# Kernel tuning notes

Measured on AMD Instinct MI355X. Metric: run time of the kernel, lower is better.

The kernel has to match this reference:

```python
import jax, jax.numpy as jnp
import numpy as np

N = 50000      # nodes
E = 500000     # edges
G = 8          # graphs in batch
IN = 128       # in_dim
HID = 64       # hidden_dim_graph == hidden_dim1
H = 2          # num_heads
C = 2          # n_classes
SLOPE = 0.2    # DGL GATConv leaky_relu negative slope


def setup_inputs() -> dict:
    key = jax.random.key(0)
    ks = jax.random.split(key, 16)
    s = lambda k, sh, fan: (jax.random.normal(k, sh, jnp.float32) / np.float32(np.sqrt(fan)))
    return {
        "h_n": jax.random.normal(ks[0], (N, IN), jnp.float32),
        "src": jax.random.randint(ks[1], (E,), 0, N),
        "dst": jax.random.randint(ks[2], (E,), 0, N),
        "graph_ids": jnp.sort(jax.random.randint(ks[3], (N,), 0, G)),
        # GATConv layer 1: fc [IN, H*HID], attn vectors [H, HID]
        "W_fc1": s(ks[4], (IN, H * HID), IN),
        "attn_l1": s(ks[5], (H, HID), HID),
        "attn_r1": s(ks[6], (H, HID), HID),
        # GATConv layer 2: fc [HID, H*HID]
        "W_fc2": s(ks[7], (HID, H * HID), HID),
        "attn_l2": s(ks[8], (H, HID), HID),
        "attn_r2": s(ks[9], (H, HID), HID),
        # gate nn: Linear(HID, 1)
        "w_gate": s(ks[10], (HID, 1), HID),
        "b_gate": jnp.zeros((1,), jnp.float32),
        # classifier MLP
        "W_c1": s(ks[11], (HID, HID), HID),
        "b_c1": jnp.zeros((HID,), jnp.float32),
        "W_c2": s(ks[12], (HID, C), HID),
        "b_c2": jnp.zeros((C,), jnp.float32),
    }


def _gat_conv(h, src, dst, W_fc, attn_l, attn_r):
    # h: [N, D_in] -> out: [N, H, HID]
    feat = (h @ W_fc).reshape(N, H, HID)
    el = (feat * attn_l).sum(-1)                 # [N, H]
    er = (feat * attn_r).sum(-1)                 # [N, H]
    e = jax.nn.leaky_relu(el[src] + er[dst], SLOPE)   # [E, H]
    # edge softmax over incoming edges per destination node
    m = jax.ops.segment_max(e, dst, num_segments=N)   # [N, H]
    ex = jnp.exp(e - m[dst])                     # [E, H]
    den = jax.ops.segment_sum(ex, dst, num_segments=N)
    alpha = ex / jnp.where(den == 0, 1.0, den)[dst]
    # message passing: sum_e alpha_e * feat[src_e]
    return jax.ops.segment_sum(alpha[:, :, None] * feat[src], dst, num_segments=N)


def _segment_softmax(x, ids, num_segments):
    m = jax.ops.segment_max(x, ids, num_segments=num_segments)
    ex = jnp.exp(x - m[ids])
    den = jax.ops.segment_sum(ex, ids, num_segments=num_segments)
    return ex / jnp.where(den == 0, 1.0, den)[ids]


def reference(h_n, src, dst, graph_ids, W_fc1, attn_l1, attn_r1, W_fc2, attn_l2,
              attn_r2, w_gate, b_gate, W_c1, b_c1, W_c2, b_c2):
    h = jax.nn.relu(_gat_conv(h_n, src, dst, W_fc1, attn_l1, attn_r1)).mean(axis=1)
    h = jax.nn.relu(_gat_conv(h, src, dst, W_fc2, attn_l2, attn_r2)).mean(axis=1)
    # global attention pooling (gate MLP + per-graph softmax + weighted sum)
    gate = (h @ w_gate + b_gate)[:, 0]                 # [N]
    a = _segment_softmax(gate, graph_ids, G)[:, None]  # [N, 1]
    hg = jax.ops.segment_sum(a * h, graph_ids, num_segments=G)  # [G, HID]
    # classifier head (dropout is identity in eval mode)
    a2 = hg @ W_c1 + b_c1
    a3 = a2 @ W_c2 + b_c2
    return (jax.nn.sigmoid(a3), a, hg)
```

## Files before the change

kernel.cpp:

```cpp
#include <hip/hip_runtime.h>
#include <hip/hip_bf16.h>

#define NN 50000
#define EE 500000
#define GG 8
#define INDIM 128
#define HID 64
#define NH 2
#define PB 32
#define TMM 32
#define CAP 32
#define NBF ((NN + TMM - 1) / TMM)
#define EPB ((EE + NBF - 1) / NBF)

typedef __bf16 bf16x4 __attribute__((ext_vector_type(4)));
typedef __bf16 bf16x8 __attribute__((ext_vector_type(8)));
typedef float  f32x4  __attribute__((ext_vector_type(4)));

__device__ inline unsigned short f2bf(float f) {
    unsigned int u = __float_as_uint(f);
    unsigned int r = (u + 0x7FFFu + ((u >> 16) & 1u)) >> 16;
    return (unsigned short)r;
}
__device__ inline unsigned int pack_bf16x2(float lo, float hi) {
    return (unsigned int)f2bf(lo) | ((unsigned int)f2bf(hi) << 16);
}
__device__ inline int lower_bound_g(const int* __restrict__ gids, int target, int N) {
    int lo = 0, hi = N;
    while (lo < hi) { int mid = (lo + hi) >> 1; if (gids[mid] < target) lo = mid + 1; else hi = mid; }
    return lo;
}

__global__ __launch_bounds__(256) void prep_kernel(
        const float* __restrict__ W1, const float* __restrict__ W2,
        unsigned short* __restrict__ Wf1, unsigned short* __restrict__ Wf2,
        unsigned int* __restrict__ zero_base) {
    int idx = blockIdx.x * 256 + threadIdx.x;
    const int ZN = GG + GG + GG * 64 + NN;
    if (idx < ZN) zero_base[idx] = 0u;
    if (idx < 128 * 128) {
        int c = idx >> 7, r = idx & 127;
        int ks = r >> 5, g = (r >> 3) & 3, e = r & 7;
        int k = ks * 32 + (e < 4 ? g * 4 + e : 16 + g * 4 + (e - 4));
        Wf1[idx] = f2bf(W1[k * 128 + c]);
    }
    if (idx < 128 * 64) {
        int c = idx >> 6, r = idx & 63;
        int ks = r >> 5, g = (r >> 3) & 3, e = r & 7;
        int k = ks * 32 + (e < 4 ? g * 4 + e : 16 + g * 4 + (e - 4));
        Wf2[idx] = f2bf(W2[k * 128 + c]);
    }
}

template <int K>
__device__ __forceinline__ void fc_core(
        char* __restrict__ smem, int n0,
        const unsigned short* __restrict__ Wf,
        const float* __restrict__ al, const float* __restrict__ ar,
        unsigned int* __restrict__ featb, float* __restrict__ el,
        float* __restrict__ er, int N) {
    char* Xb = smem;
    char* Dt = smem;
    constexpr int K2 = K * 2;
    constexpr int nks = K / 32;

    int t = threadIdx.x;
    int wv = t >> 6, l = t & 63;
    int lr = l & 15, g = l >> 4;

    bf16x8 bfr[nks][2];
#pragma unroll
    for (int ks = 0; ks < nks; ks++)
#pragma unroll
        for (int cb = 0; cb < 2; cb++) {
            int c = wv * 32 + cb * 16 + lr;
            bfr[ks][cb] = *(const bf16x8*)(Wf + (((size_t)c * nks + ks) * 4 + g) * 8);
        }

    f32x4 acc[2][2];
#pragma unroll
    for (int rb = 0; rb < 2; rb++)
#pragma unroll
        for (int cb = 0; cb < 2; cb++) acc[rb][cb] = (f32x4){0.f, 0.f, 0.f, 0.f};

#pragma unroll
    for (int ks = 0; ks < nks; ks++) {
        bf16x8 af[2];
#pragma unroll
        for (int rb = 0; rb < 2; rb++) {
            int r = rb * 16 + lr;
            const char* base = Xb + r * K2;
            int s0 = (ks * 8 + g) ^ (r & 15);
            int s1 = (ks * 8 + g + 4) ^ (r & 15);
            bf16x4 a0 = *(const bf16x4*)(base + s0 * 8);
            bf16x4 a1 = *(const bf16x4*)(base + s1 * 8);
            af[rb] = __builtin_shufflevector(a0, a1, 0, 1, 2, 3, 4, 5, 6, 7);
        }
#pragma unroll
        for (int rb = 0; rb < 2; rb++)
#pragma unroll
            for (int cb = 0; cb < 2; cb++)
                acc[rb][cb] = __builtin_amdgcn_mfma_f32_16x16x32_bf16(
                    af[rb], bfr[ks][cb], acc[rb][cb], 0, 0, 0);
    }
    __syncthreads();

#pragma unroll
    for (int rb = 0; rb < 2; rb++)
#pragma unroll
        for (int cb = 0; cb < 2; cb++)
#pragma unroll
            for (int j = 0; j < 4; j++) {
                int row = rb * 16 + 4 * g + j;
                int col = wv * 32 + cb * 16 + lr;
                int byte = (col * 2) ^ ((row & 7) << 4);
                *(unsigned short*)(Dt + row * 256 + byte) = f2bf(acc[rb][cb][j]);
            }
    __syncthreads();

#pragma unroll
    for (int u = 0; u < 2; u++) {
        int i = t + u * 256;
        int row = i >> 4, s16 = i & 15;
        uint4 v = *(const uint4*)(Dt + row * 256 + ((s16 * 16) ^ ((row & 7) << 4)));
        int gr = n0 + row;
        if (gr < N) *(uint4*)&featb[(size_t)gr * 64 + s16 * 4] = v;
    }

    {
        int r = t >> 3, p = t & 7;
        int h = p >> 2;
        const float* alh = al + h * 64 + (p & 3) * 16;
        const float* arh = ar + h * 64 + (p & 3) * 16;
        float pl = 0.f, pr = 0.f;
#pragma unroll
        for (int ii = 0; ii < 2; ii++) {
            int s16 = (p << 1) + ii;
            uint4 v = *(const uint4*)(Dt + r * 256 + ((s16 * 16) ^ ((r & 7) << 4)));
            unsigned int uu[4] = {v.x, v.y, v.z, v.w};
#pragma unroll
            for (int qq = 0; qq < 4; qq++) {
                float flo = __uint_as_float(uu[qq] << 16);
                float fhi = __uint_as_float(uu[qq] & 0xFFFF0000u);
                int cb = ii * 8 + qq * 2;
                pl += flo * alh[cb] + fhi * alh[cb + 1];
                pr += flo * arh[cb] + fhi * arh[cb + 1];
            }
        }
        pl += __shfl_xor(pl, 1, 64);
        pr += __shfl_xor(pr, 1, 64);
        pl += __shfl_xor(pl, 2, 64);
        pr += __shfl_xor(pr, 2, 64);
        int gr = n0 + r;
        if ((p & 3) == 0 && gr < N) {
            el[gr * 2 + h] = pl;
            er[gr * 2 + h] = pr;
        }
    }
}

__global__ __launch_bounds__(256, 4) void build_fc1_kernel(
        const int* __restrict__ src, const int* __restrict__ dst,
        int* __restrict__ cnt, unsigned short* __restrict__ esrc,
        const float* __restrict__ X, const unsigned short* __restrict__ Wf,
        const float* __restrict__ al, const float* __restrict__ ar,
        unsigned int* __restrict__ featb, float* __restrict__ el,
        float* __restrict__ er) {
    __shared__ __align__(16) char smem[8192];
    constexpr int K = 128, K4 = 32, XIT = 4;
    int t = threadIdx.x;
    int bid = blockIdx.x;
    int n0 = bid * TMM;

    float4 xv[XIT];
    int xrow[XIT], xslot[XIT];
#pragma unroll
    for (int u = 0; u < XIT; u++) {
        int i = t + u * 256;
        int row = i >> 5, c4 = i & (K4 - 1);
        int gr = n0 + row;
        xv[u] = make_float4(0.f, 0.f, 0.f, 0.f);
        if (gr < NN) xv[u] = *(const float4*)&X[(size_t)gr * K + (c4 << 2)];
        xrow[u] = row;
        xslot[u] = c4 ^ (row & 15);
    }

    {
        int eb = bid * EPB;
        int eend = eb + EPB;
        if (eend > EE) eend = EE;
        int dv[2], sv[2], pv[2];
        bool vv[2];
#pragma unroll
        for (int j = 0; j < 2; j++) {
            int e = eb + t + j * 256;
            vv[j] = e < eend;
            int es = vv[j] ? e : eb;
            dv[j] = dst[es];
            sv[j] = src[es];
        }
#pragma unroll
        for (int j = 0; j < 2; j++)
            if (vv[j]) pv[j] = atomicAdd(&cnt[dv[j]], 1);
#pragma unroll
        for (int j = 0; j < 2; j++)
            if (vv[j] && pv[j] < CAP)
                esrc[(size_t)dv[j] * CAP + pv[j]] = (unsigned short)sv[j];
    }

#pragma unroll
    for (int u = 0; u < XIT; u++)
        *(uint2*)(smem + xrow[u] * (K * 2) + xslot[u] * 8) =
            make_uint2(pack_bf16x2(xv[u].x, xv[u].y), pack_bf16x2(xv[u].z, xv[u].w));
    __syncthreads();

    fc_core<128>(smem, n0, Wf, al, ar, featb, el, er, NN);
}

__global__ __launch_bounds__(256, 4) void agg_fc2_kernel(
        const unsigned int* __restrict__ featb,
        const float* __restrict__ el, const float* __restrict__ er,
        const int* __restrict__ cnt, const unsigned short* __restrict__ esrc,
        const unsigned short* __restrict__ Wf,
        const float* __restrict__ al2, const float* __restrict__ ar2,
        unsigned int* __restrict__ featb2, float* __restrict__ el2,
        float* __restrict__ er2) {
    __shared__ __align__(16) char smem[8192];
    char* Xb = smem;
    int t = threadIdx.x;
    int wv = t >> 6, lane = t & 63;
    int n0 = blockIdx.x * TMM;
    int nb = n0 + wv * 8;

    int degv[8], sv8[8];
    float2 elv8[8];
#pragma unroll
    for (int j = 0; j < 8; j++) {
        int n = nb + j;
        int d = (n < NN) ? cnt[n] : 0;
        degv[j] = d > CAP ? CAP : d;
    }
#pragma unroll
    for (int j = 0; j < 8; j++) {
        int n = nb + j;
        int ns = (n < NN) ? n : 0;
        bool v = lane < degv[j];
        sv8[j] = (int)esrc[(size_t)ns * CAP + (v ? lane : 0)];
    }
#pragma unroll
    for (int j = 0; j < 8; j++) elv8[j] = ((const float2*)el)[sv8[j]];

    int q = lane >> 4;
    int l4 = lane & 15;
    int headHi = (l4 >= 8);

#pragma unroll
    for (int j = 0; j < 8; j++) {
        int n = nb + j;
        int deg = degv[j];
        float a8[8];
#pragma unroll
        for (int i = 0; i < 8; i++) a8[i] = 0.f;

        if (deg > 0) {
            float2 erv = ((const float2*)er)[n];
            bool v = lane < deg;
            int s = sv8[j];
            float2 elv = elv8[j];
            float e0 = elv.x + erv.x; e0 = e0 > 0.f ? e0 : 0.2f * e0;
            float e1 = elv.y + erv.y; e1 = e1 > 0.f ? e1 : 0.2f * e1;
            float x0 = v ? __expf(e0) : 0.f;
            float x1 = v ? __expf(e1) : 0.f;
            float d0 = x0, d1 = x1;
            for (int off = 32; off; off >>= 1) {
                d0 += __shfl_xor(d0, off, 64);
                d1 += __shfl_xor(d1, off, 64);
            }
            float a0 = x0 / d0, a1 = x1 / d1;
            for (int e = 0; e < deg; e += 4) {
                int myE = e + q;
                bool ve = myE < deg;
                int pick = ve ? myE : e;
                int se = __shfl(s, pick, 64);
                float av0 = __shfl(a0, pick, 64);
                float av1 = __shfl(a1, pick, 64);
                float a = headHi ? av1 : av0;
                if (!ve) a = 0.f;
                uint4 fv = *(const uint4*)&featb[(size_t)se * 64 + l4 * 4];
                a8[0] += a * __uint_as_float(fv.x << 16);
                a8[1] += a * __uint_as_float(fv.x & 0xFFFF0000u);
                a8[2] += a * __uint_as_float(fv.y << 16);
                a8[3] += a * __uint_as_float(fv.y & 0xFFFF0000u);
                a8[4] += a * __uint_as_float(fv.z << 16);
                a8[5] += a * __uint_as_float(fv.z & 0xFFFF0000u);
                a8[6] += a * __uint_as_float(fv.w << 16);
                a8[7] += a * __uint_as_float(fv.w & 0xFFFF0000u);
            }
        }

        float m8[8];
#pragma unroll
        for (int i = 0; i < 8; i++) {
            a8[i] += __shfl_xor(a8[i], 16, 64);
            a8[i] += __shfl_xor(a8[i], 32, 64);
            a8[i] = fmaxf(a8[i], 0.f);
            m8[i] = a8[i];
        }
#pragma unroll
        for (int i = 0; i < 8; i++) m8[i] = 0.5f * (m8[i] + __shfl_xor(m8[i], 8, 64));

        if (lane < 8) {
            int row = wv * 8 + j;
            int c4a = 2 * lane, c4b = 2 * lane + 1;
            *(uint2*)(Xb + row * 128 + ((c4a ^ (row & 15)) * 8)) =
                make_uint2(pack_bf16x2(m8[0], m8[1]), pack_bf16x2(m8[2], m8[3]));
            *(uint2*)(Xb + row * 128 + ((c4b ^ (row & 15)) * 8)) =
                make_uint2(pack_bf16x2(m8[4], m8[5]), pack_bf16x2(m8[6], m8[7]));
        }
    }
    __syncthreads();

    fc_core<64>(smem, n0, Wf, al2, ar2, featb2, el2, er2, NN);
}

__global__ void gat_agg_kernel(const unsigned int* __restrict__ featb,
                               const float* __restrict__ el,
                               const float* __restrict__ er, const int* __restrict__ cnt,
                               const unsigned short* __restrict__ esrc,
                               float* __restrict__ hout,
                               const float* __restrict__ wg, const float* __restrict__ bg,
                               float* __restrict__ gatev) {
    int wid = threadIdx.x >> 6;
    int lane = threadIdx.x & 63;
    int n = blockIdx.x * 4 + wid;
    if (n >= NN) return;
    int deg = cnt[n];
    deg = deg > CAP ? CAP : deg;
    int q = lane >> 4;
    int l4 = lane & 15;
    float a8[8];
#pragma unroll
    for (int i = 0; i < 8; i++) a8[i] = 0.f;

    if (deg > 0) {
        float2 erv = ((const float2*)er)[n];
        bool v = lane < deg;
        int s = (int)esrc[(size_t)n * CAP + (v ? lane : 0)];
        float2 elv = ((const float2*)el)[s];
        float e0 = elv.x + erv.x; e0 = e0 > 0.f ? e0 : 0.2f * e0;
        float e1 = elv.y + erv.y; e1 = e1 > 0.f ? e1 : 0.2f * e1;
        float x0 = v ? __expf(e0) : 0.f;
        float x1 = v ? __expf(e1) : 0.f;
        float d0 = x0, d1 = x1;
        for (int off = 32; off; off >>= 1) {
            d0 += __shfl_xor(d0, off, 64);
            d1 += __shfl_xor(d1, off, 64);
        }
        float a0 = x0 / d0, a1 = x1 / d1;
        int headHi = (l4 >= 8);
        for (int e = 0; e < deg; e += 4) {
            int myE = e + q;
            bool ve = myE < deg;
            int pick = ve ? myE : e;
            int se = __shfl(s, pick, 64);
            float av0 = __shfl(a0, pick, 64);
            float av1 = __shfl(a1, pick, 64);
            float a = headHi ? av1 : av0;
            if (!ve) a = 0.f;
            uint4 fv = *(const uint4*)&featb[(size_t)se * 64 + l4 * 4];
            a8[0] += a * __uint_as_float(fv.x << 16);
            a8[1] += a * __uint_as_float(fv.x & 0xFFFF0000u);
            a8[2] += a * __uint_as_float(fv.y << 16);
            a8[3] += a * __uint_as_float(fv.y & 0xFFFF0000u);
            a8[4] += a * __uint_as_float(fv.z << 16);
            a8[5] += a * __uint_as_float(fv.z & 0xFFFF0000u);
            a8[6] += a * __uint_as_float(fv.w << 16);
            a8[7] += a * __uint_as_float(fv.w & 0xFFFF0000u);
        }
    }

#pragma unroll
    for (int i = 0; i < 8; i++) {
        a8[i] += __shfl_xor(a8[i], 16, 64);
        a8[i] += __shfl_xor(a8[i], 32, 64);
        a8[i] = fmaxf(a8[i], 0.f);
    }
    float m8[8];
#pragma unroll
    for (int i = 0; i < 8; i++) m8[i] = 0.5f * (a8[i] + __shfl_xor(a8[i], 8, 64));
    if (lane < 8) {
        float4 w0 = make_float4(m8[0], m8[1], m8[2], m8[3]);
        float4 w1 = make_float4(m8[4], m8[5], m8[6], m8[7]);
        *(float4*)&hout[(size_t)n * 64 + 8 * lane] = w0;
        *(float4*)&hout[(size_t)n * 64 + 8 * lane + 4] = w1;
    }

    float val = 0.f;
    if (lane < 8) {
#pragma unroll
        for (int i = 0; i < 8; i++) val += m8[i] * wg[8 * lane + i];
    }
    val += __shfl_xor(val, 1, 64);
    val += __shfl_xor(val, 2, 64);
    val += __shfl_xor(val, 4, 64);
    if (lane == 0) gatev[n] = val + bg[0];
}

__global__ void pool_expacc_kernel(const float* __restrict__ h2, const float* __restrict__ gatev,
                                   const int* __restrict__ gids,
                                   float* __restrict__ out_a, float* __restrict__ gsum,
                                   float* __restrict__ hgacc) {
    int g = blockIdx.x / PB, b = blockIdx.x % PB;
    __shared__ int sb[2];
    int t = threadIdx.x;
    if (t == 0) { sb[0] = lower_bound_g(gids, g, NN); sb[1] = lower_bound_g(gids, g + 1, NN); }
    __syncthreads();
    int lo = sb[0], len = sb[1] - lo;
    int s = lo + (int)((long long)b * len / PB);
    int e = lo + (int)((long long)(b + 1) * len / PB);
    int sub = t >> 6, c = t & 63;
    float acc = 0.f, esum = 0.f;
    for (int n = s + sub; n < e; n += 4) {
        float ev = __expf(gatev[n]);
        if (c == 0) out_a[n] = ev;
        esum += ev;
        acc += ev * h2[(size_t)n * 64 + c];
    }
    __shared__ float sh[4][64];
    sh[sub][c] = acc;
    __syncthreads();
    if (sub == 0) atomicAdd(&hgacc[g * 64 + c], sh[0][c] + sh[1][c] + sh[2][c] + sh[3][c]);
    if (c == 0) atomicAdd(&gsum[g], esum);
}

__global__ __launch_bounds__(512) void epilogue_kernel(
        const float* __restrict__ hgacc, const float* __restrict__ gsum,
        const float* __restrict__ Wc1, const float* __restrict__ bc1,
        const float* __restrict__ Wc2, const float* __restrict__ bc2,
        const int* __restrict__ gids, float* __restrict__ out,
        float* __restrict__ out_a, float* __restrict__ out_hg) {
    int t = threadIdx.x;
    if (blockIdx.x != 0) {
        int n = (blockIdx.x - 1) * 512 + t;
        if (n < NN) {
            float sv = gsum[gids[n]];
            out_a[n] *= (sv > 0.f) ? 1.f / sv : 0.f;
        }
        return;
    }
    __shared__ float hgs[GG * 64];
    __shared__ float a2s[GG * 64];
    int g = t >> 6, c = t & 63;
    float sv = gsum[g];
    float inv = (sv > 0.f) ? 1.f / sv : 0.f;
    float hval = hgacc[t] * inv;
    hgs[t] = hval;
    out_hg[t] = hval;
    __syncthreads();
    float acc = bc1[c];
    for (int k = 0; k < 64; k++) acc += hgs[g * 64 + k] * Wc1[k * 64 + c];
    a2s[g * 64 + c] = acc;
    __syncthreads();
    if (t < GG * 2) {
        int gg = t >> 1, j = t & 1;
        float a3 = bc2[j];
        for (int k = 0; k < 64; k++) a3 += a2s[gg * 64 + k] * Wc2[k * 2 + j];
        out[t] = 1.f / (1.f + expf(-a3));
    }
}

extern "C" void kernel_launch(void* const* d_in, const int* in_sizes, int n_in,
                              void* d_out, int out_size, void* d_ws, size_t ws_size,
                              hipStream_t stream) {
    const float* h_n  = (const float*)d_in[0];
    const int*   src  = (const int*)d_in[1];
    const int*   dst  = (const int*)d_in[2];
    const int*   gids = (const int*)d_in[3];
    const float* Wfc1 = (const float*)d_in[4];
    const float* al1  = (const float*)d_in[5];
    const float* ar1  = (const float*)d_in[6];
    const float* Wfc2 = (const float*)d_in[7];
    const float* al2  = (const float*)d_in[8];
    const float* ar2  = (const float*)d_in[9];
    const float* wg   = (const float*)d_in[10];
    const float* bg   = (const float*)d_in[11];
    const float* Wc1  = (const float*)d_in[12];
    const float* bc1  = (const float*)d_in[13];
    const float* Wc2  = (const float*)d_in[14];
    const float* bc2  = (const float*)d_in[15];
    float* out = (float*)d_out;

    float* ws     = (float*)d_ws;
    unsigned int* featb = (unsigned int*)ws;
    float* el     = ws + (size_t)NN * 64;
    float* er     = el + NN * 2;
    float* hbuf   = er + NN * 2;
    float* gatev  = hbuf + (size_t)NN * 64;
    unsigned int* gmEnc = (unsigned int*)(gatev + NN);
    float* gsum   = (float*)(gmEnc + GG);
    float* hgacc  = gsum + GG;
    int*   cnt    = (int*)(hgacc + GG * 64);
    unsigned short* esrc = (unsigned short*)(cnt + NN);
    unsigned short* Wf1  = esrc + (size_t)NN * CAP;
    unsigned short* Wf2  = Wf1 + 128 * 128;
    unsigned int* featb2 = (unsigned int*)(Wf2 + 128 * 64);
    float* el2    = (float*)(featb2 + (size_t)NN * 64);
    float* er2    = el2 + NN * 2;

    const int ZN = GG + GG + GG * 64 + NN;
    prep_kernel<<<(ZN + 255) / 256, 256, 0, stream>>>(Wfc1, Wfc2, Wf1, Wf2, gmEnc);

    build_fc1_kernel<<<NBF, 256, 0, stream>>>(src, dst, cnt, esrc,
                                              h_n, Wf1, al1, ar1, featb, el, er);

    agg_fc2_kernel<<<NBF, 256, 0, stream>>>(featb, el, er, cnt, esrc,
                                            Wf2, al2, ar2, featb2, el2, er2);

    gat_agg_kernel<<<(NN + 3) / 4, 256, 0, stream>>>(featb2, el2, er2, cnt, esrc,
                                                     hbuf, wg, bg, gatev);

    pool_expacc_kernel<<<GG * PB, 256, 0, stream>>>(hbuf, gatev, gids,
                                                    out + GG * 2, gsum, hgacc);

    int nb = 1 + (NN + 511) / 512;
    epilogue_kernel<<<nb, 512, 0, stream>>>(hgacc, gsum, Wc1, bc1, Wc2, bc2, gids,
                                            out, out + GG * 2, out + GG * 2 + NN);
}
```

Baseline: 243.3 us.

## Widen agg_fc2 to 512 threads and unroll edge gather loops by two

```diff
diff --git a/kernel.cpp b/kernel.cpp
--- a/kernel.cpp
+++ b/kernel.cpp
@@ -52,7 +52,7 @@
     }
 }
 
-template <int K>
+template <int K, int NW>
 __device__ __forceinline__ void fc_core(
         char* __restrict__ smem, int n0,
         const unsigned short* __restrict__ Wf,
@@ -63,32 +63,35 @@
     char* Dt = smem;
     constexpr int K2 = K * 2;
     constexpr int nks = K / 32;
+    constexpr int NRB = (NW == 4) ? 2 : 1;
 
     int t = threadIdx.x;
     int wv = t >> 6, l = t & 63;
     int lr = l & 15, g = l >> 4;
+    int colbase = (NW == 4) ? wv * 32 : (wv & 3) * 32;
+    int rb0 = (NW == 4) ? 0 : (wv >> 2);
 
     bf16x8 bfr[nks][2];
 #pragma unroll
     for (int ks = 0; ks < nks; ks++)
 #pragma unroll
         for (int cb = 0; cb < 2; cb++) {
-            int c = wv * 32 + cb * 16 + lr;
+            int c = colbase + cb * 16 + lr;
             bfr[ks][cb] = *(const bf16x8*)(Wf + (((size_t)c * nks + ks) * 4 + g) * 8);
         }
 
-    f32x4 acc[2][2];
-#pragma unroll
-    for (int rb = 0; rb < 2; rb++)
+    f32x4 acc[NRB][2];
+#pragma unroll
+    for (int rb = 0; rb < NRB; rb++)
 #pragma unroll
         for (int cb = 0; cb < 2; cb++) acc[rb][cb] = (f32x4){0.f, 0.f, 0.f, 0.f};
 
 #pragma unroll
     for (int ks = 0; ks < nks; ks++) {
-        bf16x8 af[2];
-#pragma unroll
-        for (int rb = 0; rb < 2; rb++) {
-            int r = rb * 16 + lr;
+        bf16x8 af[NRB];
+#pragma unroll
+        for (int rb = 0; rb < NRB; rb++) {
+            int r = (rb0 + rb) * 16 + lr;
             const char* base = Xb + r * K2;
             int s0 = (ks * 8 + g) ^ (r & 15);
             int s1 = (ks * 8 + g + 4) ^ (r & 15);
@@ -97,7 +100,7 @@
             af[rb] = __builtin_shufflevector(a0, a1, 0, 1, 2, 3, 4, 5, 6, 7);
         }
 #pragma unroll
-        for (int rb = 0; rb < 2; rb++)
+        for (int rb = 0; rb < NRB; rb++)
 #pragma unroll
             for (int cb = 0; cb < 2; cb++)
                 acc[rb][cb] = __builtin_amdgcn_mfma_f32_16x16x32_bf16(
@@ -106,28 +109,27 @@
     __syncthreads();
 
 #pragma unroll
-    for (int rb = 0; rb < 2; rb++)
+    for (int rb = 0; rb < NRB; rb++)
 #pragma unroll
         for (int cb = 0; cb < 2; cb++)
 #pragma unroll
             for (int j = 0; j < 4; j++) {
-                int row = rb * 16 + 4 * g + j;
-                int col = wv * 32 + cb * 16 + lr;
+                int row = (rb0 + rb) * 16 + 4 * g + j;
+                int col = colbase + cb * 16 + lr;
                 int byte = (col * 2) ^ ((row & 7) << 4);
                 *(unsigned short*)(Dt + row * 256 + byte) = f2bf(acc[rb][cb][j]);
             }
     __syncthreads();
 
 #pragma unroll
-    for (int u = 0; u < 2; u++) {
-        int i = t + u * 256;
+    for (int i = t; i < TMM * 16; i += NW * 64) {
         int row = i >> 4, s16 = i & 15;
         uint4 v = *(const uint4*)(Dt + row * 256 + ((s16 * 16) ^ ((row & 7) << 4)));
         int gr = n0 + row;
         if (gr < N) *(uint4*)&featb[(size_t)gr * 64 + s16 * 4] = v;
     }
 
-    {
+    if (t < 256) {
         int r = t >> 3, p = t & 7;
         int h = p >> 2;
         const float* alh = al + h * 64 + (p & 3) * 16;
@@ -214,10 +216,10 @@
             make_uint2(pack_bf16x2(xv[u].x, xv[u].y), pack_bf16x2(xv[u].z, xv[u].w));
     __syncthreads();
 
-    fc_core<128>(smem, n0, Wf, al, ar, featb, el, er, NN);
-}
-
-__global__ __launch_bounds__(256, 4) void agg_fc2_kernel(
+    fc_core<128, 4>(smem, n0, Wf, al, ar, featb, el, er, NN);
+}
+
+__global__ __launch_bounds__(512, 6) void agg_fc2_kernel(
         const unsigned int* __restrict__ featb,
         const float* __restrict__ el, const float* __restrict__ er,
         const int* __restrict__ cnt, const unsigned short* __restrict__ esrc,
@@ -230,32 +232,32 @@
     int t = threadIdx.x;
     int wv = t >> 6, lane = t & 63;
     int n0 = blockIdx.x * TMM;
-    int nb = n0 + wv * 8;
-
-    int degv[8], sv8[8];
-    float2 elv8[8];
-#pragma unroll
-    for (int j = 0; j < 8; j++) {
+    int nb = n0 + wv * 4;
+
+    int degv[4], sv4[4];
+    float2 elv4[4];
+#pragma unroll
+    for (int j = 0; j < 4; j++) {
         int n = nb + j;
         int d = (n < NN) ? cnt[n] : 0;
         degv[j] = d > CAP ? CAP : d;
     }
 #pragma unroll
-    for (int j = 0; j < 8; j++) {
+    for (int j = 0; j < 4; j++) {
         int n = nb + j;
         int ns = (n < NN) ? n : 0;
         bool v = lane < degv[j];
-        sv8[j] = (int)esrc[(size_t)ns * CAP + (v ? lane : 0)];
-    }
-#pragma unroll
-    for (int j = 0; j < 8; j++) elv8[j] = ((const float2*)el)[sv8[j]];
+        sv4[j] = (int)esrc[(size_t)ns * CAP + (v ? lane : 0)];
+    }
+#pragma unroll
+    for (int j = 0; j < 4; j++) elv4[j] = ((const float2*)el)[sv4[j]];
 
     int q = lane >> 4;
     int l4 = lane & 15;
     int headHi = (l4 >= 8);
 
 #pragma unroll
-    for (int j = 0; j < 8; j++) {
+    for (int j = 0; j < 4; j++) {
         int n = nb + j;
         int deg = degv[j];
         float a8[8];
@@ -265,8 +267,8 @@
         if (deg > 0) {
             float2 erv = ((const float2*)er)[n];
             bool v = lane < deg;
-            int s = sv8[j];
-            float2 elv = elv8[j];
+            int s = sv4[j];
+            float2 elv = elv4[j];
             float e0 = elv.x + erv.x; e0 = e0 > 0.f ? e0 : 0.2f * e0;
             float e1 = elv.y + erv.y; e1 = e1 > 0.f ? e1 : 0.2f * e1;
             float x0 = v ? __expf(e0) : 0.f;
@@ -277,24 +279,38 @@
                 d1 += __shfl_xor(d1, off, 64);
             }
             float a0 = x0 / d0, a1 = x1 / d1;
-            for (int e = 0; e < deg; e += 4) {
-                int myE = e + q;
-                bool ve = myE < deg;
-                int pick = ve ? myE : e;
-                int se = __shfl(s, pick, 64);
-                float av0 = __shfl(a0, pick, 64);
-                float av1 = __shfl(a1, pick, 64);
-                float a = headHi ? av1 : av0;
-                if (!ve) a = 0.f;
-                uint4 fv = *(const uint4*)&featb[(size_t)se * 64 + l4 * 4];
-                a8[0] += a * __uint_as_float(fv.x << 16);
-                a8[1] += a * __uint_as_float(fv.x & 0xFFFF0000u);
-                a8[2] += a * __uint_as_float(fv.y << 16);
-                a8[3] += a * __uint_as_float(fv.y & 0xFFFF0000u);
-                a8[4] += a * __uint_as_float(fv.z << 16);
-                a8[5] += a * __uint_as_float(fv.z & 0xFFFF0000u);
-                a8[6] += a * __uint_as_float(fv.w << 16);
-                a8[7] += a * __uint_as_float(fv.w & 0xFFFF0000u);
+            for (int e = 0; e < deg; e += 8) {
+                int eA = e + q, eB = e + 4 + q;
+                bool vA = eA < deg, vB = eB < deg;
+                int pA = vA ? eA : e, pB = vB ? eB : e;
+                int seA = __shfl(s, pA, 64);
+                int seB = __shfl(s, pB, 64);
+                float a0A = __shfl(a0, pA, 64);
+                float a1A = __shfl(a1, pA, 64);
+                float a0B = __shfl(a0, pB, 64);
+                float a1B = __shfl(a1, pB, 64);
+                float aA = headHi ? a1A : a0A;
+                float aB = headHi ? a1B : a0B;
+                if (!vA) aA = 0.f;
+                if (!vB) aB = 0.f;
+                uint4 fvA = *(const uint4*)&featb[(size_t)seA * 64 + l4 * 4];
+                uint4 fvB = *(const uint4*)&featb[(size_t)seB * 64 + l4 * 4];
+                a8[0] += aA * __uint_as_float(fvA.x << 16);
+                a8[1] += aA * __uint_as_float(fvA.x & 0xFFFF0000u);
+                a8[2] += aA * __uint_as_float(fvA.y << 16);
+                a8[3] += aA * __uint_as_float(fvA.y & 0xFFFF0000u);
+                a8[4] += aA * __uint_as_float(fvA.z << 16);
+                a8[5] += aA * __uint_as_float(fvA.z & 0xFFFF0000u);
+                a8[6] += aA * __uint_as_float(fvA.w << 16);
+                a8[7] += aA * __uint_as_float(fvA.w & 0xFFFF0000u);
+                a8[0] += aB * __uint_as_float(fvB.x << 16);
+                a8[1] += aB * __uint_as_float(fvB.x & 0xFFFF0000u);
+                a8[2] += aB * __uint_as_float(fvB.y << 16);
+                a8[3] += aB * __uint_as_float(fvB.y & 0xFFFF0000u);
+                a8[4] += aB * __uint_as_float(fvB.z << 16);
+                a8[5] += aB * __uint_as_float(fvB.z & 0xFFFF0000u);
+                a8[6] += aB * __uint_as_float(fvB.w << 16);
+                a8[7] += aB * __uint_as_float(fvB.w & 0xFFFF0000u);
             }
         }
 
@@ -310,7 +326,7 @@
         for (int i = 0; i < 8; i++) m8[i] = 0.5f * (m8[i] + __shfl_xor(m8[i], 8, 64));
 
         if (lane < 8) {
-            int row = wv * 8 + j;
+            int row = wv * 4 + j;
             int c4a = 2 * lane, c4b = 2 * lane + 1;
             *(uint2*)(Xb + row * 128 + ((c4a ^ (row & 15)) * 8)) =
                 make_uint2(pack_bf16x2(m8[0], m8[1]), pack_bf16x2(m8[2], m8[3]));
@@ -320,16 +336,17 @@
     }
     __syncthreads();
 
-    fc_core<64>(smem, n0, Wf, al2, ar2, featb2, el2, er2, NN);
-}
-
-__global__ void gat_agg_kernel(const unsigned int* __restrict__ featb,
-                               const float* __restrict__ el,
-                               const float* __restrict__ er, const int* __restrict__ cnt,
-                               const unsigned short* __restrict__ esrc,
-                               float* __restrict__ hout,
-                               const float* __restrict__ wg, const float* __restrict__ bg,
-                               float* __restrict__ gatev) {
+    fc_core<64, 8>(smem, n0, Wf, al2, ar2, featb2, el2, er2, NN);
+}
+
+__global__ __launch_bounds__(256) void gat_agg_kernel(
+        const unsigned int* __restrict__ featb,
+        const float* __restrict__ el,
+        const float* __restrict__ er, const int* __restrict__ cnt,
+        const unsigned short* __restrict__ esrc,
+        float* __restrict__ hout,
+        const float* __restrict__ wg, const float* __restrict__ bg,
+        float* __restrict__ gatev) {
     int wid = threadIdx.x >> 6;
     int lane = threadIdx.x & 63;
     int n = blockIdx.x * 4 + wid;
@@ -358,24 +375,38 @@
         }
         float a0 = x0 / d0, a1 = x1 / d1;
         int headHi = (l4 >= 8);
-        for (int e = 0; e < deg; e += 4) {
-            int myE = e + q;
-            bool ve = myE < deg;
-            int pick = ve ? myE : e;
-            int se = __shfl(s, pick, 64);
-            float av0 = __shfl(a0, pick, 64);
-            float av1 = __shfl(a1, pick, 64);
-            float a = headHi ? av1 : av0;
-            if (!ve) a = 0.f;
-            uint4 fv = *(const uint4*)&featb[(size_t)se * 64 + l4 * 4];
-            a8[0] += a * __uint_as_float(fv.x << 16);
-            a8[1] += a * __uint_as_float(fv.x & 0xFFFF0000u);
-            a8[2] += a * __uint_as_float(fv.y << 16);
-            a8[3] += a * __uint_as_float(fv.y & 0xFFFF0000u);
-            a8[4] += a * __uint_as_float(fv.z << 16);
-            a8[5] += a * __uint_as_float(fv.z & 0xFFFF0000u);
-            a8[6] += a * __uint_as_float(fv.w << 16);
-            a8[7] += a * __uint_as_float(fv.w & 0xFFFF0000u);
+        for (int e = 0; e < deg; e += 8) {
+            int eA = e + q, eB = e + 4 + q;
+            bool vA = eA < deg, vB = eB < deg;
+            int pA = vA ? eA : e, pB = vB ? eB : e;
+            int seA = __shfl(s, pA, 64);
+            int seB = __shfl(s, pB, 64);
+            float a0A = __shfl(a0, pA, 64);
+            float a1A = __shfl(a1, pA, 64);
+            float a0B = __shfl(a0, pB, 64);
+            float a1B = __shfl(a1, pB, 64);
+            float aA = headHi ? a1A : a0A;
+            float aB = headHi ? a1B : a0B;
+            if (!vA) aA = 0.f;
+            if (!vB) aB = 0.f;
+            uint4 fvA = *(const uint4*)&featb[(size_t)seA * 64 + l4 * 4];
+            uint4 fvB = *(const uint4*)&featb[(size_t)seB * 64 + l4 * 4];
+            a8[0] += aA * __uint_as_float(fvA.x << 16);
+            a8[1] += aA * __uint_as_float(fvA.x & 0xFFFF0000u);
+            a8[2] += aA * __uint_as_float(fvA.y << 16);
+            a8[3] += aA * __uint_as_float(fvA.y & 0xFFFF0000u);
+            a8[4] += aA * __uint_as_float(fvA.z << 16);
+            a8[5] += aA * __uint_as_float(fvA.z & 0xFFFF0000u);
+            a8[6] += aA * __uint_as_float(fvA.w << 16);
+            a8[7] += aA * __uint_as_float(fvA.w & 0xFFFF0000u);
+            a8[0] += aB * __uint_as_float(fvB.x << 16);
+            a8[1] += aB * __uint_as_float(fvB.x & 0xFFFF0000u);
+            a8[2] += aB * __uint_as_float(fvB.y << 16);
+            a8[3] += aB * __uint_as_float(fvB.y & 0xFFFF0000u);
+            a8[4] += aB * __uint_as_float(fvB.z << 16);
+            a8[5] += aB * __uint_as_float(fvB.z & 0xFFFF0000u);
+            a8[6] += aB * __uint_as_float(fvB.w << 16);
+            a8[7] += aB * __uint_as_float(fvB.w & 0xFFFF0000u);
         }
     }
 
@@ -513,7 +544,7 @@
     build_fc1_kernel<<<NBF, 256, 0, stream>>>(src, dst, cnt, esrc,
                                               h_n, Wf1, al1, ar1, featb, el, er);
 
-    agg_fc2_kernel<<<NBF, 256, 0, stream>>>(featb, el, er, cnt, esrc,
+    agg_fc2_kernel<<<NBF, 512, 0, stream>>>(featb, el, er, cnt, esrc,
                                             Wf2, al2, ar2, featb2, el2, er2);
 
     gat_agg_kernel<<<(NN + 3) / 4, 256, 0, stream>>>(featb2, el2, er2, cnt, esrc,
```

Measured after the change: 238.8 us. No clear change (-1.8%).
